# Kernel tuning notes

Hardware: AMD Instinct MI355X
Metric: run time of the kernel (lower is better)

The kernel has to match this reference:

```python
import jax, jax.numpy as jnp
import numpy as np

TEMPERATURE = 0.1
NEG_INF = -1e30  # finite sentinel so masked logsumexp has zero (not NaN) gradient


def setup_inputs() -> dict:
    key = jax.random.key(0)
    k1, k2, k3 = jax.random.split(key, 3)
    N, D = 8192, 512          # flattened (batch * TRs) trials, feature dim
    NUM_CLASSES = 3           # vigilance states
    return {
        "objs_feats": jax.random.normal(k1, (N, D), dtype=jnp.float32),
        "objs_labels": jax.random.randint(k2, (N,), 0, NUM_CLASSES, dtype=jnp.int32),
        "bad_tr": jax.random.randint(k3, (N,), 0, 2, dtype=jnp.int32),
    }


def reference(objs_feats, objs_labels, bad_tr):
    # Faithful vectorization of SetCriterion.contrastive_loss_batch_without_break.
    N = objs_feats.shape[0]
    f = objs_feats / jnp.linalg.norm(objs_feats, axis=-1, keepdims=True)
    S = (f @ f.T) / TEMPERATURE                      # [N, N] cosine-sim logits

    valid = bad_tr == 0                              # [N]
    same = objs_labels[:, None] == objs_labels[None, :]
    eye = jnp.eye(N, dtype=bool)
    neg_mask = valid[None, :] & (~same)              # [N, N] negatives per anchor
    pos_mask = valid[None, :] & same & (~eye)        # [N, N] positives per anchor

    has_neg = neg_mask.any(axis=1)
    has_pos = pos_mask.any(axis=1)
    processed = valid & has_neg                      # anchors the loop doesn't `continue` past

    # logsumexp over negatives of each anchor row
    neg_lse = jax.nn.logsumexp(jnp.where(neg_mask, S, NEG_INF), axis=1)  # [N]

    # anchors WITH positives: CE over rows [S[i,p], S[i, negs...]] with target 0,
    # averaged over positives p -> mean_p( logaddexp(S[i,p], neg_lse_i) - S[i,p] )
    ce_per_pos = jnp.logaddexp(S, neg_lse[:, None]) - S                  # [N, N]
    pos_cnt = pos_mask.sum(axis=1)
    loss_with_pos = jnp.where(pos_mask, ce_per_pos, 0.0).sum(axis=1) / jnp.maximum(pos_cnt, 1)

    # anchors WITHOUT positives: pos logit is the constant 1/temperature
    inv_t = jnp.float32(1.0 / TEMPERATURE)
    loss_no_pos = jnp.logaddexp(inv_t, neg_lse) - inv_t

    per_anchor = jnp.where(has_pos, loss_with_pos, loss_no_pos)
    total = jnp.where(processed, per_anchor, 0.0).sum()
    # valid_obj_cnt starts at 1; no-pos anchors net to 0 (−1 then +1)
    count = 1 + (processed & has_pos).sum()
    return total / count.astype(total.dtype)
```

## Files before the change

### kernel.cpp

```cpp
#include <hip/hip_runtime.h>

typedef __bf16 bf16x8 __attribute__((ext_vector_type(8)));
typedef __bf16 bf16x4 __attribute__((ext_vector_type(4)));
typedef float f32x4 __attribute__((ext_vector_type(4)));

#define SLOTW 260

#define GLOAD_LDS16(g, l)                                                      \
  __builtin_amdgcn_global_load_lds(                                            \
      (const __attribute__((address_space(1))) void*)(g),                      \
      (__attribute__((address_space(3))) void*)(l), 16, 0, 0)

__global__ __launch_bounds__(1024) void k_scan(
    const int* __restrict__ labels, const int* __restrict__ bad,
    unsigned char* __restrict__ code, int* __restrict__ dst,
    int* __restrict__ hdr, __bf16* __restrict__ fng,
    unsigned char* __restrict__ gcode, float* __restrict__ out, int Nv,
    int Dv) {
  const int t = threadIdx.x;
  const int per = Nv >> 10;
  const int base = t * per;
  unsigned char lc[8];
  int cnt[3] = {0, 0, 0};
  for (int k = 0; k < per; ++k) {
    const int r = base + k;
    const unsigned char c =
        (bad[r] == 0) ? (unsigned char)labels[r] : (unsigned char)255;
    lc[k] = c;
    code[r] = c;
    if (c <= 2) cnt[c]++;
  }
  __shared__ int s0[1024], s1[1024], s2[1024];
  s0[t] = cnt[0];
  s1[t] = cnt[1];
  s2[t] = cnt[2];
  __syncthreads();
  for (int off = 1; off < 1024; off <<= 1) {
    const int a0 = (t >= off) ? s0[t - off] : 0;
    const int a1 = (t >= off) ? s1[t - off] : 0;
    const int a2 = (t >= off) ? s2[t - off] : 0;
    __syncthreads();
    s0[t] += a0;
    s1[t] += a1;
    s2[t] += a2;
    __syncthreads();
  }
  const int C0 = s0[1023], C1 = s1[1023], C2 = s2[1023];
  int run[3];
  run[0] = s0[t] - cnt[0];
  run[1] = C0 + s1[t] - cnt[1];
  run[2] = C0 + C1 + s2[t] - cnt[2];
  for (int k = 0; k < per; ++k) {
    const int c = lc[k];
    dst[base + k] = (c <= 2) ? run[c]++ : -1;
  }
  const int M = C0 + C1 + C2;
  const int Mpad = (M + 127) & ~127;
  if (t == 0) {
    const int NTv = Mpad >> 7;
    hdr[0] = M;
    hdr[1] = Mpad;
    hdr[2] = NTv;
    hdr[3] = NTv * (NTv + 1) / 2;
    hdr[4] = C0;
    hdr[5] = C1;
    hdr[6] = C2;
    int count = 1;
    if (C0 >= 2 && M > C0) count += C0;
    if (C1 >= 2 && M > C1) count += C1;
    if (C2 >= 2 && M > C2) count += C2;
    hdr[7] = count;
    out[0] = 0.f;
  }
  for (int i = M + t; i < Mpad; i += 1024) gcode[i] = 255;
  const int nv4 = (Mpad - M) * (Dv >> 3);
  float4* fp = (float4*)(fng + (size_t)M * Dv);
  const float4 z = {0.f, 0.f, 0.f, 0.f};
  for (int i = t; i < nv4; i += 1024) fp[i] = z;
}

__global__ __launch_bounds__(128) void k_norm(const float* __restrict__ X,
                                              const unsigned char* __restrict__
                                                  code,
                                              const int* __restrict__ dst,
                                              __bf16* __restrict__ fng,
                                              unsigned char* __restrict__ gcode,
                                              int Dv) {
  const int row = blockIdx.x;
  const unsigned char c = code[row];
  if (c > 2) return;
  const int g = dst[row];
  const int t = threadIdx.x;
  const float4* xr = (const float4*)(X + (size_t)row * Dv);
  float ss = 0.f;
  const int nv4 = Dv >> 2;
  for (int idx = t; idx < nv4; idx += 128) {
    float4 v = xr[idx];
    ss += v.x * v.x + v.y * v.y + v.z * v.z + v.w * v.w;
  }
#pragma unroll
  for (int off = 32; off; off >>= 1) ss += __shfl_down(ss, off);
  __shared__ float sred[2];
  if ((t & 63) == 0) sred[t >> 6] = ss;
  __syncthreads();
  const float inv = 1.0f / sqrtf(sred[0] + sred[1]);
  const int nv8 = Dv >> 3;
  for (int idx = t; idx < nv8; idx += 128) {
    const float4 v0 = xr[idx * 2];
    const float4 v1 = xr[idx * 2 + 1];
    bf16x8 o;
    o[0] = (__bf16)(v0.x * inv);
    o[1] = (__bf16)(v0.y * inv);
    o[2] = (__bf16)(v0.z * inv);
    o[3] = (__bf16)(v0.w * inv);
    o[4] = (__bf16)(v1.x * inv);
    o[5] = (__bf16)(v1.y * inv);
    o[6] = (__bf16)(v1.z * inv);
    o[7] = (__bf16)(v1.w * inv);
    *(bf16x8*)(fng + (size_t)g * Dv + idx * 8) = o;
  }
  if (t == 0) gcode[g] = c;
}

__device__ __forceinline__ void tri_decode(int blk, int NT, int& bi, int& bj) {
  int b = 0, rem = blk, span = NT;
  while (rem >= span) {
    rem -= span;
    b++;
    span--;
  }
  bi = b;
  bj = b + rem;
}

__device__ __forceinline__ bool tile_overlap(const unsigned char* gcode,
                                             size_t sA, size_t rowB) {
  const int la0 = gcode[sA], la1 = gcode[sA + 63];
  const int lb0 = gcode[rowB], lb1 = gcode[rowB + 127];
  const int hiA = la1 > 2 ? 2 : la1;
  const int hiB = lb1 > 2 ? 2 : lb1;
  const int lo = la0 > lb0 ? la0 : lb0;
  const int hi = hiA < hiB ? hiA : hiB;
  return (la0 <= 2) && (lb0 <= 2) && (lo <= hi);
}

__global__ __launch_bounds__(256, 6) void k_p1(
    const __bf16* __restrict__ fng, const unsigned char* __restrict__ gcode,
    const int* __restrict__ hdr, float* __restrict__ P,
    _Float16* __restrict__ Sc, int Dv) {
  const int NTv = hdr[2];
  if ((int)blockIdx.x >= hdr[3]) return;
  int bi, bj;
  tri_decode(blockIdx.x, NTv, bi, bj);
  const int h = blockIdx.y;
  const size_t sA = (size_t)bi * 128 + h * 64;
  const size_t rowB = (size_t)bj * 128;
  __shared__ __align__(16) __bf16 As[2][64 * 32];
  __shared__ __align__(16) __bf16 Bs[2][128 * 32];

  const int t = threadIdx.x;
  const int lane = t & 63;
  const int wave = t >> 6;
  const int quad = lane >> 4;
  const int l16 = lane & 15;
  const int wr = (wave >> 1) * 32;
  const int wc = (wave & 1) * 64;
  const int r4 = t >> 2, q4 = t & 3;
  const int r4b = (t + 256) >> 2, q4b = (t + 256) & 3;

  f32x4 acc[2][4] = {};
  auto stage = [&](int k0, int b) {
    GLOAD_LDS16(fng + (sA + r4) * Dv + k0 + q4 * 8,
                &As[b][(size_t)wave * 64 * 8]);
    GLOAD_LDS16(fng + (rowB + r4) * Dv + k0 + q4 * 8,
                &Bs[b][(size_t)wave * 64 * 8]);
    GLOAD_LDS16(fng + (rowB + r4b) * Dv + k0 + q4b * 8,
                &Bs[b][(size_t)(256 + wave * 64) * 8]);
  };
  stage(0, 0);
  int buf = 0;
  for (int k0 = 0; k0 < Dv; k0 += 32) {
    __syncthreads();
    if (k0 + 32 < Dv) stage(k0 + 32, buf ^ 1);
    bf16x8 af[2], bfv[4];
#pragma unroll
    for (int mi = 0; mi < 2; ++mi)
      af[mi] = *(const bf16x8*)&As[buf][(wr + mi * 16 + l16) * 32 + quad * 8];
#pragma unroll
    for (int ni = 0; ni < 4; ++ni)
      bfv[ni] = *(const bf16x8*)&Bs[buf][(wc + ni * 16 + l16) * 32 + quad * 8];
#pragma unroll
    for (int mi = 0; mi < 2; ++mi)
#pragma unroll
      for (int ni = 0; ni < 4; ++ni)
        acc[mi][ni] = __builtin_amdgcn_mfma_f32_16x16x32_bf16(
            af[mi], bfv[ni], acc[mi][ni], 0, 0, 0);
    buf ^= 1;
  }

  unsigned char ca[8], cb[4];
#pragma unroll
  for (int mi = 0; mi < 2; ++mi)
#pragma unroll
    for (int r = 0; r < 4; ++r)
      ca[mi * 4 + r] = gcode[sA + wr + mi * 16 + quad * 4 + r];
#pragma unroll
  for (int ni = 0; ni < 4; ++ni) cb[ni] = gcode[rowB + wc + ni * 16 + l16];
  const bool ov = tile_overlap(gcode, sA, rowB);
  _Float16* St = Sc + ((size_t)blockIdx.x * 2 + h) * 8192;

  float rowsum[8] = {};
  float colsum[4] = {};
#pragma unroll
  for (int mi = 0; mi < 2; ++mi)
#pragma unroll
    for (int ni = 0; ni < 4; ++ni)
#pragma unroll
      for (int r = 0; r < 4; ++r) {
        const float s = acc[mi][ni][r] * 10.0f;
        const float ex = __expf(s);
        const int a = ca[mi * 4 + r], b = cb[ni];
        const bool diff = a != b;
        rowsum[mi * 4 + r] += (b <= 2 && diff) ? ex : 0.f;
        colsum[ni] += (a <= 2 && diff) ? ex : 0.f;
        if (ov)
          St[(wr + mi * 16 + quad * 4 + r) * 128 + wc + ni * 16 + l16] =
              (_Float16)s;
      }
#pragma unroll
  for (int off = 1; off < 16; off <<= 1)
#pragma unroll
    for (int k = 0; k < 8; ++k) rowsum[k] += __shfl_xor(rowsum[k], off);
  if (l16 == 0)
#pragma unroll
    for (int k = 0; k < 8; ++k) {
      const size_t base =
          (sA + wr + (k >> 2) * 16 + quad * 4 + (k & 3)) * SLOTW + bj * 4;
      P[base + h * 2 + (wave & 1)] = rowsum[k];
      P[base + (1 - h) * 2 + (wave & 1)] = 0.f;
    }
  if (bi != bj) {
#pragma unroll
    for (int off = 16; off < 64; off <<= 1)
#pragma unroll
      for (int ni = 0; ni < 4; ++ni) colsum[ni] += __shfl_xor(colsum[ni], off);
    if (quad == 0)
#pragma unroll
      for (int ni = 0; ni < 4; ++ni)
        P[(rowB + wc + ni * 16 + l16) * SLOTW + bi * 4 + h * 2 + (wave >> 1)] =
            colsum[ni];
  }
}

__global__ __launch_bounds__(256) void k_red(const float* __restrict__ P,
                                             float* __restrict__ out,
                                             const int* __restrict__ hdr,
                                             int Nv) {
  const int g = blockIdx.x * 256 + threadIdx.x;
  if (g >= Nv || g >= hdr[1]) return;
  const int ns = hdr[2] * 4;
  float s = 0.f;
  const float4* p = (const float4*)(P + (size_t)g * SLOTW);
  for (int k = 0; k < (ns >> 2); ++k) {
    const float4 v = p[k];
    s += v.x + v.y + v.z + v.w;
  }
  out[g] = s;
}

__global__ __launch_bounds__(256) void k_p2(
    const unsigned char* __restrict__ gcode, const int* __restrict__ hdr,
    const float* __restrict__ E, float* __restrict__ P2,
    const _Float16* __restrict__ Sc) {
  const int NTv = hdr[2];
  if ((int)blockIdx.x >= hdr[3]) return;
  int bi, bj;
  tri_decode(blockIdx.x, NTv, bi, bj);
  const int h = blockIdx.y;
  const size_t sA = (size_t)bi * 128 + h * 64;
  const size_t rowB = (size_t)bj * 128;
  const int t = threadIdx.x;
  const bool diag = (bi == bj);

  if (!tile_overlap(gcode, sA, rowB)) {
    if (t < 64) {
      const size_t base = (sA + t) * SLOTW + bj * 4;
      P2[base] = 0.f;
      P2[base + 1] = 0.f;
      P2[base + 2] = 0.f;
      P2[base + 3] = 0.f;
    } else if (t < 192 && !diag) {
      const size_t base = (rowB + t - 64) * SLOTW + bi * 4 + h * 2;
      P2[base] = 0.f;
      P2[base + 1] = 0.f;
    }
    return;
  }

  const _Float16* St = Sc + ((size_t)blockIdx.x * 2 + h) * 8192;
  const int l8 = t & 15;
  unsigned char cb[8];
  float eB[8];
  {
    const uint2 cv = *(const uint2*)(gcode + rowB + l8 * 8);
    const unsigned char* cp = (const unsigned char*)&cv;
#pragma unroll
    for (int e = 0; e < 8; ++e) cb[e] = cp[e];
    const float4 e0 = *(const float4*)(E + rowB + l8 * 8);
    const float4 e1 = *(const float4*)(E + rowB + l8 * 8 + 4);
    eB[0] = e0.x; eB[1] = e0.y; eB[2] = e0.z; eB[3] = e0.w;
    eB[4] = e1.x; eB[5] = e1.y; eB[6] = e1.z; eB[7] = e1.w;
  }
  float colsum[8] = {};
#pragma unroll
  for (int k = 0; k < 4; ++k) {
    const int row = k * 16 + (t >> 4);
    const int a = gcode[sA + row];
    const float eA = E[sA + row];
    const float4 sv = *(const float4*)(St + row * 128 + l8 * 8);
    const _Float16* hp = (const _Float16*)&sv;
    float rsum = 0.f;
#pragma unroll
    for (int e = 0; e < 8; ++e) {
      const int col = l8 * 8 + e;
      const float em = __expf(-(float)hp[e]);
      const bool pos =
          (a == cb[e]) && (cb[e] <= 2) && !(diag && (row + h * 64) == col);
      rsum += pos ? __logf(1.f + eA * em) : 0.f;
      colsum[e] += pos ? __logf(1.f + eB[e] * em) : 0.f;
    }
#pragma unroll
    for (int off = 1; off < 16; off <<= 1) rsum += __shfl_xor(rsum, off);
    if (l8 == 0) {
      const size_t base = (sA + row) * SLOTW + bj * 4;
      P2[base + h * 2] = rsum;
      P2[base + h * 2 + 1] = 0.f;
      P2[base + (1 - h) * 2] = 0.f;
      P2[base + (1 - h) * 2 + 1] = 0.f;
    }
  }
  __shared__ float colpart[128 * 17];
#pragma unroll
  for (int e = 0; e < 8; ++e) colpart[(l8 * 8 + e) * 17 + (t >> 4)] = colsum[e];
  __syncthreads();
  if (t < 128 && !diag) {
    float cs = 0.f;
#pragma unroll
    for (int i = 0; i < 16; ++i) cs += colpart[t * 17 + i];
    const size_t base = (rowB + t) * SLOTW + bi * 4 + h * 2;
    P2[base] = cs;
    P2[base + 1] = 0.f;
  }
}

__global__ __launch_bounds__(256) void k_fin(const float* __restrict__ P2,
                                             const float* __restrict__ E,
                                             const unsigned char* __restrict__
                                                 gcode,
                                             const int* __restrict__ hdr,
                                             float* __restrict__ out) {
  const int g = blockIdx.x * 256 + threadIdx.x;
  const int t = threadIdx.x;
  float contrib = 0.f;
  if (g < hdr[1]) {
    const int l = gcode[g];
    if (l <= 2) {
      const int c0 = hdr[4], c1 = hdr[5], c2 = hdr[6];
      const int vt = c0 + c1 + c2;
      const int cmy = (l == 0) ? c0 : ((l == 1) ? c1 : c2);
      if (vt - cmy > 0) {
        const int pos_cnt = cmy - 1;
        if (pos_cnt > 0) {
          const int ns = hdr[2] * 4;
          float s = 0.f;
          const float4* p = (const float4*)(P2 + (size_t)g * SLOTW);
          for (int k = 0; k < (ns >> 2); ++k) {
            const float4 v = p[k];
            s += v.x + v.y + v.z + v.w;
          }
          contrib = s / (float)pos_cnt;
        } else {
          contrib = __logf(1.f + E[g] * __expf(-10.0f));
        }
      }
    }
  }
#pragma unroll
  for (int off = 32; off; off >>= 1) contrib += __shfl_down(contrib, off);
  __shared__ float sd[4];
  if ((t & 63) == 0) sd[t >> 6] = contrib;
  __syncthreads();
  if (t == 0) {
    const float tot = sd[0] + sd[1] + sd[2] + sd[3];
    atomicAdd(out, tot / (float)hdr[7]);
  }
}

extern "C" void kernel_launch(void* const* d_in, const int* in_sizes, int n_in,
                              void* d_out, int out_size, void* d_ws,
                              size_t ws_size, hipStream_t stream) {
  const float* X = (const float*)d_in[0];
  const int* labels = (const int*)d_in[1];
  const int* bad = (const int*)d_in[2];
  const int Nv = in_sizes[1];
  const int Dv = in_sizes[0] / Nv;

  size_t off = 0;
  auto alloc = [&](size_t bytes) -> void* {
    size_t p = (off + 255) & ~(size_t)255;
    off = p + bytes;
    return (void*)((char*)d_ws + p);
  };
  const int NT = Nv / 128;
  const int ntri_max = NT * (NT + 1) / 2;
  __bf16* fng = (__bf16*)alloc((size_t)Nv * Dv * 2);
  float* P = (float*)alloc((size_t)Nv * SLOTW * 4);
  float* P2 = (float*)alloc((size_t)Nv * SLOTW * 4);
  _Float16* Sc = (_Float16*)alloc((size_t)ntri_max * 2 * 8192 * 2);
  float* E = (float*)alloc((size_t)Nv * 4);
  int* dst = (int*)alloc((size_t)Nv * 4);
  unsigned char* code = (unsigned char*)alloc((size_t)Nv);
  unsigned char* gcode = (unsigned char*)alloc((size_t)Nv);
  int* hdr = (int*)alloc(64);
  if (off > ws_size) return;

  k_scan<<<1, 1024, 0, stream>>>(labels, bad, code, dst, hdr, fng, gcode,
                                 (float*)d_out, Nv, Dv);
  k_norm<<<Nv, 128, 0, stream>>>(X, code, dst, fng, gcode, Dv);
  dim3 gp(ntri_max, 2);
  k_p1<<<gp, 256, 0, stream>>>(fng, gcode, hdr, P, Sc, Dv);
  k_red<<<(Nv + 255) / 256, 256, 0, stream>>>(P, E, hdr, Nv);
  k_p2<<<gp, 256, 0, stream>>>(gcode, hdr, E, P2, Sc);
  k_fin<<<(Nv + 255) / 256, 256, 0, stream>>>(P2, E, gcode, hdr,
                                              (float*)d_out);
}
```

Baseline: 148.4 us.

## Merge half-tile p1 blocks into 512-thread 128x128 blocks with XCD-aware remap

k_p1 now runs one 512-thread block per 128x128 triangular tile instead of two 256-thread half-tile blocks, so the B tile is loaded into LDS once and shared by both halves, halving B global traffic. Block IDs are remapped so consecutive tiles are grouped per XCD (bid&7 chunking), which is meant to improve L2 locality. The k_scan prefix sum uses wave shuffles plus a 16-entry serial pass in place of a 10-step LDS scan, and k_norm gets a single-pass path for D=512 that reads each row once. The Sc layout must match what k_p2 reads (tile*16384 + h*8192), and the larger block plus the launch_bounds occupancy hint may raise register pressure.

```diff
diff --git a/kernel.cpp b/kernel.cpp
--- a/kernel.cpp
+++ b/kernel.cpp
@@ -18,6 +18,7 @@
     unsigned char* __restrict__ gcode, float* __restrict__ out, int Nv,
     int Dv) {
   const int t = threadIdx.x;
+  const int lane = t & 63, wv = t >> 6;
   const int per = Nv >> 10;
   const int base = t * per;
   unsigned char lc[8];
@@ -30,26 +31,45 @@
     code[r] = c;
     if (c <= 2) cnt[c]++;
   }
-  __shared__ int s0[1024], s1[1024], s2[1024];
-  s0[t] = cnt[0];
-  s1[t] = cnt[1];
-  s2[t] = cnt[2];
+  int inc0 = cnt[0], inc1 = cnt[1], inc2 = cnt[2];
+#pragma unroll
+  for (int off = 1; off < 64; off <<= 1) {
+    const int a = __shfl_up(inc0, off);
+    const int b = __shfl_up(inc1, off);
+    const int c = __shfl_up(inc2, off);
+    if (lane >= off) {
+      inc0 += a;
+      inc1 += b;
+      inc2 += c;
+    }
+  }
+  __shared__ int wt[16][3], wo[17][3];
+  if (lane == 63) {
+    wt[wv][0] = inc0;
+    wt[wv][1] = inc1;
+    wt[wv][2] = inc2;
+  }
   __syncthreads();
-  for (int off = 1; off < 1024; off <<= 1) {
-    const int a0 = (t >= off) ? s0[t - off] : 0;
-    const int a1 = (t >= off) ? s1[t - off] : 0;
-    const int a2 = (t >= off) ? s2[t - off] : 0;
-    __syncthreads();
-    s0[t] += a0;
-    s1[t] += a1;
-    s2[t] += a2;
-    __syncthreads();
-  }
-  const int C0 = s0[1023], C1 = s1[1023], C2 = s2[1023];
+  if (t == 0) {
+    int s0 = 0, s1 = 0, s2 = 0;
+    for (int w = 0; w < 16; ++w) {
+      wo[w][0] = s0;
+      wo[w][1] = s1;
+      wo[w][2] = s2;
+      s0 += wt[w][0];
+      s1 += wt[w][1];
+      s2 += wt[w][2];
+    }
+    wo[16][0] = s0;
+    wo[16][1] = s1;
+    wo[16][2] = s2;
+  }
+  __syncthreads();
+  const int C0 = wo[16][0], C1 = wo[16][1], C2 = wo[16][2];
   int run[3];
-  run[0] = s0[t] - cnt[0];
-  run[1] = C0 + s1[t] - cnt[1];
-  run[2] = C0 + C1 + s2[t] - cnt[2];
+  run[0] = wo[wv][0] + inc0 - cnt[0];
+  run[1] = C0 + wo[wv][1] + inc1 - cnt[1];
+  run[2] = C0 + C1 + wo[wv][2] + inc2 - cnt[2];
   for (int k = 0; k < per; ++k) {
     const int c = lc[k];
     dst[base + k] = (c <= 2) ? run[c]++ : -1;
@@ -92,15 +112,32 @@
   const int g = dst[row];
   const int t = threadIdx.x;
   const float4* xr = (const float4*)(X + (size_t)row * Dv);
+  const int nv4 = Dv >> 2;
+  __shared__ float sred[2];
+  if (nv4 == 128) {
+    const float4 v = xr[t];
+    float ss = v.x * v.x + v.y * v.y + v.z * v.z + v.w * v.w;
+#pragma unroll
+    for (int off = 32; off; off >>= 1) ss += __shfl_down(ss, off);
+    if ((t & 63) == 0) sred[t >> 6] = ss;
+    __syncthreads();
+    const float inv = 1.0f / sqrtf(sred[0] + sred[1]);
+    bf16x4 o;
+    o[0] = (__bf16)(v.x * inv);
+    o[1] = (__bf16)(v.y * inv);
+    o[2] = (__bf16)(v.z * inv);
+    o[3] = (__bf16)(v.w * inv);
+    *(bf16x4*)(fng + (size_t)g * Dv + t * 4) = o;
+    if (t == 0) gcode[g] = c;
+    return;
+  }
   float ss = 0.f;
-  const int nv4 = Dv >> 2;
   for (int idx = t; idx < nv4; idx += 128) {
     float4 v = xr[idx];
     ss += v.x * v.x + v.y * v.y + v.z * v.z + v.w * v.w;
   }
 #pragma unroll
   for (int off = 32; off; off >>= 1) ss += __shfl_down(ss, off);
-  __shared__ float sred[2];
   if ((t & 63) == 0) sred[t >> 6] = ss;
   __syncthreads();
   const float inv = 1.0f / sqrtf(sred[0] + sred[1]);
@@ -134,8 +171,9 @@
 }
 
 __device__ __forceinline__ bool tile_overlap(const unsigned char* gcode,
-                                             size_t sA, size_t rowB) {
-  const int la0 = gcode[sA], la1 = gcode[sA + 63];
+                                             size_t sA, int lastA,
+                                             size_t rowB) {
+  const int la0 = gcode[sA], la1 = gcode[sA + lastA];
   const int lb0 = gcode[rowB], lb1 = gcode[rowB + 127];
   const int hiA = la1 > 2 ? 2 : la1;
   const int hiB = lb1 > 2 ? 2 : lb1;
@@ -144,18 +182,23 @@
   return (la0 <= 2) && (lb0 <= 2) && (lo <= hi);
 }
 
-__global__ __launch_bounds__(256, 6) void k_p1(
+__global__ __launch_bounds__(512, 6) void k_p1(
     const __bf16* __restrict__ fng, const unsigned char* __restrict__ gcode,
     const int* __restrict__ hdr, float* __restrict__ P,
     _Float16* __restrict__ Sc, int Dv) {
   const int NTv = hdr[2];
-  if ((int)blockIdx.x >= hdr[3]) return;
+  const int ntri = hdr[3];
+  int bid = blockIdx.x;
+  if (bid >= ntri) return;
+  {
+    const int q = ntri >> 3, r = ntri & 7, x = bid & 7, o = bid >> 3;
+    bid = (x < r ? x * (q + 1) : r * (q + 1) + (x - r) * q) + o;
+  }
   int bi, bj;
-  tri_decode(blockIdx.x, NTv, bi, bj);
-  const int h = blockIdx.y;
-  const size_t sA = (size_t)bi * 128 + h * 64;
+  tri_decode(bid, NTv, bi, bj);
+  const size_t sA = (size_t)bi * 128;
   const size_t rowB = (size_t)bj * 128;
-  __shared__ __align__(16) __bf16 As[2][64 * 32];
+  __shared__ __align__(16) __bf16 As[2][128 * 32];
   __shared__ __align__(16) __bf16 Bs[2][128 * 32];
 
   const int t = threadIdx.x;
@@ -166,7 +209,6 @@
   const int wr = (wave >> 1) * 32;
   const int wc = (wave & 1) * 64;
   const int r4 = t >> 2, q4 = t & 3;
-  const int r4b = (t + 256) >> 2, q4b = (t + 256) & 3;
 
   f32x4 acc[2][4] = {};
   auto stage = [&](int k0, int b) {
@@ -174,8 +216,6 @@
                 &As[b][(size_t)wave * 64 * 8]);
     GLOAD_LDS16(fng + (rowB + r4) * Dv + k0 + q4 * 8,
                 &Bs[b][(size_t)wave * 64 * 8]);
-    GLOAD_LDS16(fng + (rowB + r4b) * Dv + k0 + q4b * 8,
-                &Bs[b][(size_t)(256 + wave * 64) * 8]);
   };
   stage(0, 0);
   int buf = 0;
@@ -206,8 +246,8 @@
       ca[mi * 4 + r] = gcode[sA + wr + mi * 16 + quad * 4 + r];
 #pragma unroll
   for (int ni = 0; ni < 4; ++ni) cb[ni] = gcode[rowB + wc + ni * 16 + l16];
-  const bool ov = tile_overlap(gcode, sA, rowB);
-  _Float16* St = Sc + ((size_t)blockIdx.x * 2 + h) * 8192;
+  const bool ov = tile_overlap(gcode, sA, 127, rowB);
+  _Float16* St = Sc + (size_t)bid * 16384;
 
   float rowsum[8] = {};
   float colsum[4] = {};
@@ -236,8 +276,8 @@
     for (int k = 0; k < 8; ++k) {
       const size_t base =
           (sA + wr + (k >> 2) * 16 + quad * 4 + (k & 3)) * SLOTW + bj * 4;
-      P[base + h * 2 + (wave & 1)] = rowsum[k];
-      P[base + (1 - h) * 2 + (wave & 1)] = 0.f;
+      P[base + (wave & 1)] = rowsum[k];
+      P[base + 2 + (wave & 1)] = 0.f;
     }
   if (bi != bj) {
 #pragma unroll
@@ -247,7 +287,7 @@
     if (quad == 0)
 #pragma unroll
       for (int ni = 0; ni < 4; ++ni)
-        P[(rowB + wc + ni * 16 + l16) * SLOTW + bi * 4 + h * 2 + (wave >> 1)] =
+        P[(rowB + wc + ni * 16 + l16) * SLOTW + bi * 4 + (wave >> 1)] =
             colsum[ni];
   }
 }
@@ -282,7 +322,7 @@
   const int t = threadIdx.x;
   const bool diag = (bi == bj);
 
-  if (!tile_overlap(gcode, sA, rowB)) {
+  if (!tile_overlap(gcode, sA, 63, rowB)) {
     if (t < 64) {
       const size_t base = (sA + t) * SLOTW + bj * 4;
       P2[base] = 0.f;
@@ -427,9 +467,9 @@
   k_scan<<<1, 1024, 0, stream>>>(labels, bad, code, dst, hdr, fng, gcode,
                                  (float*)d_out, Nv, Dv);
   k_norm<<<Nv, 128, 0, stream>>>(X, code, dst, fng, gcode, Dv);
+  k_p1<<<ntri_max, 512, 0, stream>>>(fng, gcode, hdr, P, Sc, Dv);
+  k_red<<<(Nv + 255) / 256, 256, 0, stream>>>(P, E, hdr, Nv);
   dim3 gp(ntri_max, 2);
-  k_p1<<<gp, 256, 0, stream>>>(fng, gcode, hdr, P, Sc, Dv);
-  k_red<<<(Nv + 255) / 256, 256, 0, stream>>>(P, E, hdr, Nv);
   k_p2<<<gp, 256, 0, stream>>>(gcode, hdr, E, P2, Sc);
   k_fin<<<(Nv + 255) / 256, 256, 0, stream>>>(P2, E, gcode, hdr,
                                               (float*)d_out);
```

Result: faster. 140.5 us (-5.4%).
